# Kernel tuning notes

Measured on AMD Instinct MI355X. Metric: run time of the kernel, lower is better.

Reference implementation:

```python
import jax, jax.numpy as jnp
import numpy as np
import math

B, L, CS, CZ, H = 1, 256, 384, 128, 8
DH_S = CS // H
NEG = -1e9

def _ln(x, g, b):
    m = x.mean(-1, keepdims=True)
    v = ((x - m) ** 2).mean(-1, keepdims=True)
    return (x - m) / jnp.sqrt(v + 1e-5) * g + b

def _mha(x, mask, w_in, b_in, w_out, b_out):
    # torch nn.MultiheadAttention (batch_first) with packed in_proj [3C,C]
    N, Lx, C = x.shape
    dh = C // H
    qkv = x @ w_in.T + b_in
    q, k, v = jnp.split(qkv, 3, axis=-1)
    q = q.reshape(N, Lx, H, dh)
    k = k.reshape(N, Lx, H, dh)
    v = v.reshape(N, Lx, H, dh)
    logits = jnp.einsum('nlhd,nmhd->nhlm', q, k) / math.sqrt(dh)
    logits = jnp.where(mask[:, None, None, :], logits, NEG)
    a = jax.nn.softmax(logits, axis=-1)
    o = jnp.einsum('nhlm,nmhd->nlhd', a, v).reshape(N, Lx, C)
    return o @ w_out.T + b_out

def _forward(s, z, s_norm_g, s_norm_b, z_norm_g, z_norm_b, wq, bq, wk, bk, wv, bv, wzb, bzb, wo, bo, sff_w1, sff_b1, sff_w2, sff_b2, pz_norm_g, pz_norm_b, row_in_w, row_in_b, row_out_w, row_out_b, col_in_w, col_in_b, col_out_w, col_out_b, szi_w, szj_w, zff_w1, zff_b1, zff_w2, zff_b2, pair_mask):
    Bx, Lx, _ = s.shape
    # --- pair-bias attention on s ---
    sn = _ln(s, s_norm_g, s_norm_b)
    zn = _ln(z, z_norm_g, z_norm_b)
    q = (sn @ wq + bq).reshape(Bx, Lx, H, DH_S)
    k = (sn @ wk + bk).reshape(Bx, Lx, H, DH_S)
    v = (sn @ wv + bv).reshape(Bx, Lx, H, DH_S)
    logits = jnp.einsum('blhd,bmhd->bhlm', q, k) / math.sqrt(DH_S)
    logits = logits + jnp.transpose(zn @ wzb + bzb, (0, 3, 1, 2))
    logits = jnp.where(pair_mask[:, None, :, :], logits, NEG)
    attn = jax.nn.softmax(logits, axis=-1)
    o = jnp.einsum('bhlm,bmhd->blhd', attn, v).reshape(Bx, Lx, CS)
    s = s + o @ wo + bo
    # --- s feedforward ---
    sn = _ln(s, s_norm_g, s_norm_b)
    s = s + jax.nn.gelu(sn @ sff_w1 + sff_b1, approximate=False) @ sff_w2 + sff_b2
    # --- pair row/col attention ---
    znp = _ln(z, pz_norm_g, pz_norm_b)
    z_row = znp.reshape(Bx * Lx, Lx, CZ)
    row_out = _mha(z_row, pair_mask.reshape(Bx * Lx, Lx), row_in_w, row_in_b, row_out_w, row_out_b).reshape(Bx, Lx, Lx, CZ)
    z_col = jnp.transpose(znp, (0, 2, 1, 3)).reshape(Bx * Lx, Lx, CZ)
    col_mask = jnp.transpose(pair_mask, (0, 2, 1)).reshape(Bx * Lx, Lx)
    col_out = _mha(z_col, col_mask, col_in_w, col_in_b, col_out_w, col_out_b).reshape(Bx, Lx, Lx, CZ)
    col_out = jnp.transpose(col_out, (0, 2, 1, 3))
    z = z + row_out + col_out
    # --- outer-sum update from s ---
    sn = _ln(s, s_norm_g, s_norm_b)
    z = z + (sn @ szi_w)[:, :, None, :] + (sn @ szj_w)[:, None, :, :]
    # --- z feedforward (reuses z_norm as in source) ---
    znf = _ln(z, z_norm_g, z_norm_b)
    z = z + jax.nn.gelu(znf @ zff_w1 + zff_b1, approximate=False) @ zff_w2 + zff_b2
    return s, z

def setup_inputs():
    ks = iter(jax.random.split(jax.random.key(0), 64))
    def rn(sh, sc=0.02):
        return jax.random.normal(next(ks), sh, jnp.float32) * sc
    d = {}
    d['s'] = jax.random.normal(next(ks), (B, L, CS), jnp.float32)
    d['z'] = jax.random.normal(next(ks), (B, L, L, CZ), jnp.float32)
    d['pair_mask'] = jnp.ones((B, L, L), dtype=bool)
    d['s_norm_g'] = jnp.ones((CS,), jnp.float32); d['s_norm_b'] = jnp.zeros((CS,), jnp.float32)
    d['z_norm_g'] = jnp.ones((CZ,), jnp.float32); d['z_norm_b'] = jnp.zeros((CZ,), jnp.float32)
    d['wq'] = rn((CS, CS)); d['bq'] = jnp.zeros((CS,), jnp.float32)
    d['wk'] = rn((CS, CS)); d['bk'] = jnp.zeros((CS,), jnp.float32)
    d['wv'] = rn((CS, CS)); d['bv'] = jnp.zeros((CS,), jnp.float32)
    d['wzb'] = rn((CZ, H)); d['bzb'] = jnp.zeros((H,), jnp.float32)
    d['wo'] = rn((CS, CS)); d['bo'] = jnp.zeros((CS,), jnp.float32)
    d['sff_w1'] = rn((CS, 4 * CS)); d['sff_b1'] = jnp.zeros((4 * CS,), jnp.float32)
    d['sff_w2'] = rn((4 * CS, CS)); d['sff_b2'] = jnp.zeros((CS,), jnp.float32)
    d['pz_norm_g'] = jnp.ones((CZ,), jnp.float32); d['pz_norm_b'] = jnp.zeros((CZ,), jnp.float32)
    d['row_in_w'] = rn((3 * CZ, CZ)); d['row_in_b'] = jnp.zeros((3 * CZ,), jnp.float32)
    d['row_out_w'] = rn((CZ, CZ)); d['row_out_b'] = jnp.zeros((CZ,), jnp.float32)
    d['col_in_w'] = rn((3 * CZ, CZ)); d['col_in_b'] = jnp.zeros((3 * CZ,), jnp.float32)
    d['col_out_w'] = rn((CZ, CZ)); d['col_out_b'] = jnp.zeros((CZ,), jnp.float32)
    d['szi_w'] = rn((CS, CZ)); d['szj_w'] = rn((CS, CZ))
    d['zff_w1'] = rn((CZ, 4 * CZ)); d['zff_b1'] = jnp.zeros((4 * CZ,), jnp.float32)
    d['zff_w2'] = rn((4 * CZ, CZ)); d['zff_b2'] = jnp.zeros((CZ,), jnp.float32)
    return d

def reference(s, z, pair_mask, s_norm_g, s_norm_b, z_norm_g, z_norm_b, wq, bq, wk, bk, wv, bv, wzb, bzb, wo, bo, sff_w1, sff_b1, sff_w2, sff_b2, pz_norm_g, pz_norm_b, row_in_w, row_in_b, row_out_w, row_out_b, col_in_w, col_in_b, col_out_w, col_out_b, szi_w, szj_w, zff_w1, zff_b1, zff_w2, zff_b2):
    return _forward(s, z, s_norm_g, s_norm_b, z_norm_g, z_norm_b, wq, bq, wk, bk, wv, bv, wzb, bzb, wo, bo, sff_w1, sff_b1, sff_w2, sff_b2, pz_norm_g, pz_norm_b, row_in_w, row_in_b, row_out_w, row_out_b, col_in_w, col_in_b, col_out_w, col_out_b, szi_w, szj_w, zff_w1, zff_b1, zff_w2, zff_b2, pair_mask)
```

## Files before the change

kernel.cpp:

```cpp
#include <hip/hip_runtime.h>
#include <math.h>

#define LL 256
#define CSD 384
#define CZD 128
#define HNUM 8
#define DHS 48
#define DHZ 16

typedef __bf16 bf16_t;
typedef bf16_t bf16x8 __attribute__((ext_vector_type(8)));
typedef float f32x4 __attribute__((ext_vector_type(4)));
typedef float f32x16 __attribute__((ext_vector_type(16)));

template <typename OUT>
__global__ void ln_kernel(const float* __restrict__ x, const float* __restrict__ g,
                          const float* __restrict__ b, OUT* __restrict__ y, int W) {
    size_t row = blockIdx.x;
    int t = threadIdx.x;
    float v = x[row * (size_t)W + t];
    float s = v, s2 = v * v;
#pragma unroll
    for (int o = 32; o > 0; o >>= 1) { s += __shfl_down(s, o); s2 += __shfl_down(s2, o); }
    __shared__ float sh[8], sh2[8];
    int w = t >> 6, nw = W >> 6;
    if ((t & 63) == 0) { sh[w] = s; sh2[w] = s2; }
    __syncthreads();
    if (t == 0) {
        float a = 0, a2 = 0;
        for (int i = 0; i < nw; i++) { a += sh[i]; a2 += sh2[i]; }
        sh[0] = a; sh2[0] = a2;
    }
    __syncthreads();
    float mean = sh[0] / W;
    float var = sh2[0] / W - mean * mean;
    y[row * (size_t)W + t] = (OUT)((v - mean) * rsqrtf(var + 1e-5f) * g[t] + b[t]);
}

__global__ __launch_bounds__(256) void zlnbias_kernel(
        const float* __restrict__ z, const float* __restrict__ zng, const float* __restrict__ znb,
        const float* __restrict__ pzg, const float* __restrict__ pzb,
        const float* __restrict__ wzb, const float* __restrict__ bzb,
        float* __restrict__ bias, bf16_t* __restrict__ znp) {
    __shared__ float swzb[1024];
    int tid = threadIdx.x;
    *(float4*)&swzb[tid * 4] = *(const float4*)&wzb[tid * 4];
    __syncthreads();
    int p = blockIdx.x * 32 + (tid >> 3);
    int g = tid & 7, c0 = g * 16;
    const float* row = z + (size_t)p * 128 + c0;
    float v[16];
#pragma unroll
    for (int i = 0; i < 4; i++) *(float4*)&v[i * 4] = *(const float4*)(row + i * 4);
    float s = 0.f, s2 = 0.f;
#pragma unroll
    for (int c = 0; c < 16; c++) { s += v[c]; s2 += v[c] * v[c]; }
#pragma unroll
    for (int m = 1; m <= 4; m <<= 1) { s += __shfl_xor(s, m); s2 += __shfl_xor(s2, m); }
    float mean = s * 0.0078125f;
    float var = s2 * 0.0078125f - mean * mean;
    float rstd = rsqrtf(var + 1e-5f);
    float zg[16], zb[16], pg[16], pb[16];
#pragma unroll
    for (int i = 0; i < 4; i++) {
        *(float4*)&zg[i * 4] = *(const float4*)(zng + c0 + i * 4);
        *(float4*)&zb[i * 4] = *(const float4*)(znb + c0 + i * 4);
        *(float4*)&pg[i * 4] = *(const float4*)(pzg + c0 + i * 4);
        *(float4*)&pb[i * 4] = *(const float4*)(pzb + c0 + i * 4);
    }
    float pr[8] = {0.f, 0.f, 0.f, 0.f, 0.f, 0.f, 0.f, 0.f};
    bf16_t ob[16];
#pragma unroll
    for (int c = 0; c < 16; c++) {
        float nrm = (v[c] - mean) * rstd;
        ob[c] = (bf16_t)(nrm * pg[c] + pb[c]);
        float zn = nrm * zg[c] + zb[c];
        float4 w0 = *(const float4*)&swzb[(c0 + c) * 8];
        float4 w1 = *(const float4*)&swzb[(c0 + c) * 8 + 4];
        pr[0] += zn * w0.x; pr[1] += zn * w0.y; pr[2] += zn * w0.z; pr[3] += zn * w0.w;
        pr[4] += zn * w1.x; pr[5] += zn * w1.y; pr[6] += zn * w1.z; pr[7] += zn * w1.w;
    }
    bf16_t* orow = znp + (size_t)p * 128 + c0;
    *(uint4*)orow = *(uint4*)&ob[0];
    *(uint4*)(orow + 8) = *(uint4*)&ob[8];
#pragma unroll
    for (int m = 1; m <= 4; m <<= 1)
#pragma unroll
        for (int h = 0; h < 8; h++) pr[h] += __shfl_xor(pr[h], m);
    if (g == 0) {
#pragma unroll
        for (int h = 0; h < 8; h++) bias[(size_t)h * 65536 + p] = pr[h] + bzb[h];
    }
}

__global__ __launch_bounds__(256) void outerln_kernel(
        float* __restrict__ z, const float* __restrict__ ab,
        const float* __restrict__ zng, const float* __restrict__ znb,
        bf16_t* __restrict__ znp) {
    int tid = threadIdx.x;
    int p = blockIdx.x * 32 + (tid >> 3);
    int g = tid & 7, c0 = g * 16;
    int i = p >> 8, j = p & 255;
    float* row = z + (size_t)p * 128 + c0;
    float v[16];
#pragma unroll
    for (int q = 0; q < 4; q++) {
        float4 xv = *(const float4*)(row + q * 4);
        float4 av = *(const float4*)(ab + (size_t)i * 256 + c0 + q * 4);
        float4 bv = *(const float4*)(ab + (size_t)j * 256 + 128 + c0 + q * 4);
        v[q * 4 + 0] = xv.x + av.x + bv.x;
        v[q * 4 + 1] = xv.y + av.y + bv.y;
        v[q * 4 + 2] = xv.z + av.z + bv.z;
        v[q * 4 + 3] = xv.w + av.w + bv.w;
        *(float4*)(row + q * 4) = *(float4*)&v[q * 4];
    }
    float s = 0.f, s2 = 0.f;
#pragma unroll
    for (int c = 0; c < 16; c++) { s += v[c]; s2 += v[c] * v[c]; }
#pragma unroll
    for (int m = 1; m <= 4; m <<= 1) { s += __shfl_xor(s, m); s2 += __shfl_xor(s2, m); }
    float mean = s * 0.0078125f;
    float var = s2 * 0.0078125f - mean * mean;
    float rstd = rsqrtf(var + 1e-5f);
    float zg[16], zb[16];
#pragma unroll
    for (int q = 0; q < 4; q++) {
        *(float4*)&zg[q * 4] = *(const float4*)(zng + c0 + q * 4);
        *(float4*)&zb[q * 4] = *(const float4*)(znb + c0 + q * 4);
    }
    bf16_t ob[16];
#pragma unroll
    for (int c = 0; c < 16; c++) ob[c] = (bf16_t)((v[c] - mean) * rstd * zg[c] + zb[c]);
    bf16_t* orow = znp + (size_t)p * 128 + c0;
    *(uint4*)orow = *(uint4*)&ob[0];
    *(uint4*)(orow + 8) = *(uint4*)&ob[8];
}

__global__ void sattn_kernel(const float* __restrict__ qkv, const float* __restrict__ bias,
                             bf16_t* __restrict__ o) {
    int l = blockIdx.x, h = blockIdx.y;
    int m = threadIdx.x;
    const float* qr = qkv + (size_t)l * 1152 + h * DHS;
    const float* kr = qkv + (size_t)m * 1152 + 384 + h * DHS;
    float acc = 0.f;
#pragma unroll
    for (int d = 0; d < DHS; d++) acc += qr[d] * kr[d];
    acc = acc * 0.14433756729740643f + bias[(size_t)h * 65536 + l * 256 + m];

    __shared__ float attn[256];
    __shared__ float redm[4], reds[4];
    float x = acc;
#pragma unroll
    for (int off = 32; off > 0; off >>= 1) x = fmaxf(x, __shfl_down(x, off));
    if ((m & 63) == 0) redm[m >> 6] = x;
    __syncthreads();
    float mx = fmaxf(fmaxf(redm[0], redm[1]), fmaxf(redm[2], redm[3]));
    float p = __expf(acc - mx);
    float ss = p;
#pragma unroll
    for (int off = 32; off > 0; off >>= 1) ss += __shfl_down(ss, off);
    if ((m & 63) == 0) reds[m >> 6] = ss;
    __syncthreads();
    float sum = reds[0] + reds[1] + reds[2] + reds[3];
    attn[m] = p / sum;
    __syncthreads();
    if (m < DHS) {
        float a = 0.f;
        for (int j = 0; j < 256; j++) a += attn[j] * qkv[(size_t)j * 1152 + 768 + h * DHS + m];
        o[(size_t)l * CSD + h * DHS + m] = (bf16_t)a;
    }
}

__global__ __launch_bounds__(256) void pattn_mfma_kernel(const bf16_t* __restrict__ qkv,
                                                         bf16_t* __restrict__ o) {
    int n = blockIdx.x, h = blockIdx.y;
    int tid = threadIdx.x;
    __shared__ bf16_t Qs[256 * 24];
    __shared__ bf16_t Ks[256 * 24];
    __shared__ bf16_t Vt[32 * 264];
    __shared__ bf16_t Ps[4][32 * 72];

    {
        const bf16_t* row = qkv + ((size_t)n * 256 + tid) * 384 + h * 16;
        uint4 q0 = *(const uint4*)(row);
        uint4 q1 = *(const uint4*)(row + 8);
        uint4 k0 = *(const uint4*)(row + 128);
        uint4 k1 = *(const uint4*)(row + 136);
        uint4 v0 = *(const uint4*)(row + 256);
        uint4 v1 = *(const uint4*)(row + 264);
        *(uint4*)&Qs[tid * 24] = q0; *(uint4*)&Qs[tid * 24 + 8] = q1;
        *(uint4*)&Ks[tid * 24] = k0; *(uint4*)&Ks[tid * 24 + 8] = k1;
        bf16_t vv[16];
        *(uint4*)&vv[0] = v0; *(uint4*)&vv[8] = v1;
#pragma unroll
        for (int d = 0; d < 16; d++) Vt[d * 264 + tid] = vv[d];
        Vt[16 * 264 + tid] = (bf16_t)1.0f;
    }
    __syncthreads();

    int wv = tid >> 6, lane = tid & 63;
    int l5 = lane >> 5, l31 = lane & 31;
    bf16_t* P = &Ps[wv][0];
    const f32x16 zero16 = {0.f,0.f,0.f,0.f,0.f,0.f,0.f,0.f,0.f,0.f,0.f,0.f,0.f,0.f,0.f,0.f};

    for (int chunk = 0; chunk < 2; chunk++) {
        int q0i = wv * 64 + chunk * 32;
        bf16x8 aq = *(const bf16x8*)&Qs[(q0i + l31) * 24 + l5 * 8];
        f32x16 oacc = zero16;
        for (int kt = 0; kt < 4; kt++) {
#pragma unroll
            for (int ct2 = 0; ct2 < 2; ct2++) {
                int ct = kt * 2 + ct2;
                bf16x8 kb = *(const bf16x8*)&Ks[(ct * 32 + l31) * 24 + l5 * 8];
                f32x16 s = __builtin_amdgcn_mfma_f32_32x32x16_bf16(aq, kb, zero16, 0, 0, 0);
#pragma unroll
                for (int r = 0; r < 16; r++) {
                    float p = __expf(0.25f * s[r]);
                    int prow = (r & 3) + 8 * (r >> 2) + 4 * l5;
                    P[prow * 72 + ct2 * 32 + l31] = (bf16_t)p;
                }
            }
#pragma unroll
            for (int st = 0; st < 4; st++) {
                bf16x8 pa = *(const bf16x8*)&P[l31 * 72 + st * 16 + l5 * 8];
                bf16x8 vb = *(const bf16x8*)&Vt[l31 * 264 + kt * 64 + st * 16 + l5 * 8];
                oacc = __builtin_amdgcn_mfma_f32_32x32x16_bf16(pa, vb, oacc, 0, 0, 0);
            }
        }
#pragma unroll
        for (int r = 0; r < 16; r++) {
            float v = oacc[r];
            float sum = __shfl(v, (lane & 32) + 16, 64);
            int prow = (r & 3) + 8 * (r >> 2) + 4 * l5;
            if (l31 < 16)
                o[((size_t)n * 256 + q0i + prow) * CZD + h * 16 + l31] = (bf16_t)(v / sum);
        }
    }
}

template <int RES, int ACT, int OUTBF>
__global__ __launch_bounds__(256) void sgemm_kernel(const bf16_t* __restrict__ A,
                                                    const bf16_t* __restrict__ Bw,
                                                    const float* __restrict__ bias,
                                                    const float* __restrict__ R,
                                                    float* __restrict__ C,
                                                    bf16_t* __restrict__ Cb,
                                                    int M, int N, int K) {
    __shared__ bf16_t As[2][64 * 72];
    __shared__ bf16_t Bs[2][64 * 72];
    int tid = threadIdx.x;
    int bm = blockIdx.y * 64, bn = blockIdx.x * 64;
    int lane = tid & 63, wv = tid >> 6;
    int wm = (wv >> 1) * 32, wn = (wv & 1) * 32;
    int lrow = lane & 15, lchunk = lane >> 4;
    int r0 = tid >> 2, c0 = (tid & 3) * 16;

    f32x4 acc[2][2];
#pragma unroll
    for (int i = 0; i < 2; i++)
#pragma unroll
        for (int j = 0; j < 2; j++) acc[i][j] = (f32x4){0.f, 0.f, 0.f, 0.f};

    size_t sa = (size_t)(bm + r0) * K + c0;
    size_t sb = (size_t)(bn + r0) * K + c0;
    uint4 a0 = *(const uint4*)(A + sa);
    uint4 a1 = *(const uint4*)(A + sa + 8);
    uint4 b0 = *(const uint4*)(Bw + sb);
    uint4 b1 = *(const uint4*)(Bw + sb + 8);

    int iters = K >> 6;
    for (int it = 0; it < iters; it++) {
        bf16_t* Aw = &As[it & 1][0];
        bf16_t* Bww = &Bs[it & 1][0];
        *(uint4*)&Aw[r0 * 72 + c0] = a0;
        *(uint4*)&Aw[r0 * 72 + c0 + 8] = a1;
        *(uint4*)&Bww[r0 * 72 + c0] = b0;
        *(uint4*)&Bww[r0 * 72 + c0 + 8] = b1;
        __syncthreads();
        if (it + 1 < iters) {
            size_t oa = sa + (size_t)(it + 1) * 64;
            size_t ob = sb + (size_t)(it + 1) * 64;
            a0 = *(const uint4*)(A + oa);
            a1 = *(const uint4*)(A + oa + 8);
            b0 = *(const uint4*)(Bw + ob);
            b1 = *(const uint4*)(Bw + ob + 8);
        }
#pragma unroll
        for (int ki = 0; ki < 2; ki++) {
            bf16x8 af[2], bfr[2];
#pragma unroll
            for (int f = 0; f < 2; f++) {
                af[f] = *(const bf16x8*)&Aw[(wm + f * 16 + lrow) * 72 + ki * 32 + lchunk * 8];
                bfr[f] = *(const bf16x8*)&Bww[(wn + f * 16 + lrow) * 72 + ki * 32 + lchunk * 8];
            }
#pragma unroll
            for (int fi = 0; fi < 2; fi++)
#pragma unroll
                for (int fj = 0; fj < 2; fj++)
                    acc[fi][fj] = __builtin_amdgcn_mfma_f32_16x16x32_bf16(af[fi], bfr[fj], acc[fi][fj], 0, 0, 0);
        }
        __syncthreads();
    }
#pragma unroll
    for (int fi = 0; fi < 2; fi++) {
#pragma unroll
        for (int i = 0; i < 4; i++) {
            int gm = bm + wm + fi * 16 + lchunk * 4 + i;
            size_t crow = (size_t)gm * N;
#pragma unroll
            for (int fj = 0; fj < 2; fj++) {
                int gn = bn + wn + fj * 16 + lrow;
                float val = acc[fi][fj][i];
                if (bias) val += bias[gn];
                if (ACT == 1) val = 0.5f * val * (1.f + erff(val * 0.70710678118654752f));
                if (RES == 2) val += R[crow + gn];
                if (OUTBF) Cb[crow + gn] = (bf16_t)val;
                else C[crow + gn] = val;
            }
        }
    }
}

template <int APERM, int RES, int ACT, int OUTBF>
__global__ __launch_bounds__(256) void mgemm_kernel(const bf16_t* __restrict__ A,
                                                    const bf16_t* __restrict__ Bw,
                                                    const float* __restrict__ bias,
                                                    const float* __restrict__ R,
                                                    float* __restrict__ C,
                                                    bf16_t* __restrict__ Cb,
                                                    int M, int N, int K) {
    __shared__ bf16_t As[128 * 40];
    __shared__ bf16_t Bs[128 * 40];
    int tid = threadIdx.x;
    int bm = blockIdx.y * 128, bn = blockIdx.x * 128;
    int lane = tid & 63, wvid = tid >> 6;
    int wm = (wvid >> 1) * 64, wn = (wvid & 1) * 64;
    int lrow = lane & 15, lchunk = lane >> 4;

    f32x4 acc[4][4];
#pragma unroll
    for (int i = 0; i < 4; i++)
#pragma unroll
        for (int j = 0; j < 4; j++) acc[i][j] = (f32x4){0.f, 0.f, 0.f, 0.f};

    int r0 = tid >> 2, c0 = tid & 3;
    int ra0 = bm + r0, ra1 = bm + r0 + 64;
    if (APERM) {
        ra0 = ((ra0 & 255) << 8) | (ra0 >> 8);
        ra1 = ((ra1 & 255) << 8) | (ra1 >> 8);
    }
    size_t sa0 = (size_t)ra0 * K, sa1 = (size_t)ra1 * K;
    size_t sb0 = (size_t)(bn + r0) * K, sb1 = (size_t)(bn + r0 + 64) * K;

    for (int k0 = 0; k0 < K; k0 += 32) {
        uint4 va0 = *(const uint4*)(A + sa0 + k0 + c0 * 8);
        uint4 va1 = *(const uint4*)(A + sa1 + k0 + c0 * 8);
        uint4 vb0 = *(const uint4*)(Bw + sb0 + k0 + c0 * 8);
        uint4 vb1 = *(const uint4*)(Bw + sb1 + k0 + c0 * 8);
        __syncthreads();
        *(uint4*)&As[r0 * 40 + c0 * 8] = va0;
        *(uint4*)&As[(r0 + 64) * 40 + c0 * 8] = va1;
        *(uint4*)&Bs[r0 * 40 + c0 * 8] = vb0;
        *(uint4*)&Bs[(r0 + 64) * 40 + c0 * 8] = vb1;
        __syncthreads();
        bf16x8 af[4], bfr[4];
#pragma unroll
        for (int f = 0; f < 4; f++) {
            af[f] = *(const bf16x8*)&As[(wm + f * 16 + lrow) * 40 + lchunk * 8];
            bfr[f] = *(const bf16x8*)&Bs[(wn + f * 16 + lrow) * 40 + lchunk * 8];
        }
#pragma unroll
        for (int fi = 0; fi < 4; fi++)
#pragma unroll
            for (int fj = 0; fj < 4; fj++)
                acc[fi][fj] = __builtin_amdgcn_mfma_f32_16x16x32_bf16(af[fi], bfr[fj], acc[fi][fj], 0, 0, 0);
    }
#pragma unroll
    for (int fi = 0; fi < 4; fi++) {
#pragma unroll
        for (int i = 0; i < 4; i++) {
            int gm = bm + wm + fi * 16 + lchunk * 4 + i;
            size_t crow = (size_t)gm * N;
#pragma unroll
            for (int fj = 0; fj < 4; fj++) {
                int gn = bn + wn + fj * 16 + lrow;
                float val = acc[fi][fj][i];
                if (bias) val += bias[gn];
                if (ACT == 1) val = 0.5f * val * (1.f + erff(val * 0.70710678118654752f));
                if (RES == 1) val += C[crow + gn];
                else if (RES == 2) val += R[crow + gn];
                if (OUTBF) Cb[crow + gn] = (bf16_t)val;
                else C[crow + gn] = val;
            }
        }
    }
}

struct PrepArgs {
    const float *wq, *wk, *wv, *wo, *sffw1, *sffw2, *szi, *szj, *zffw1, *zffw2;
    const float *rinw, *cinw, *routw, *coutw, *bq, *bk, *bv;
    bf16_t *wqkv, *wwo, *wsf1, *wsf2, *wszij, *wzf1, *wzf2;
    bf16_t *wrin, *wcin, *wrout, *wcout;
    float* biasqkv;
};
__device__ inline void dev_trans(const float* in, bf16_t* out, int i, int N, int K) {
    int k = i / N, n = i % N;
    out[(size_t)n * K + k] = (bf16_t)in[i];
}
__global__ void prep_kernel(PrepArgs a) {
    int i = blockIdx.x * 256 + threadIdx.x;
    if (i < 147456) { dev_trans(a.wq, a.wqkv, i, 384, 384); return; }
    i -= 147456;
    if (i < 147456) { dev_trans(a.wk, a.wqkv + 384 * 384, i, 384, 384); return; }
    i -= 147456;
    if (i < 147456) { dev_trans(a.wv, a.wqkv + 768 * 384, i, 384, 384); return; }
    i -= 147456;
    if (i < 147456) { dev_trans(a.wo, a.wwo, i, 384, 384); return; }
    i -= 147456;
    if (i < 589824) { dev_trans(a.sffw1, a.wsf1, i, 1536, 384); return; }
    i -= 589824;
    if (i < 589824) { dev_trans(a.sffw2, a.wsf2, i, 384, 1536); return; }
    i -= 589824;
    if (i < 49152) { dev_trans(a.szi, a.wszij, i, 128, 384); return; }
    i -= 49152;
    if (i < 49152) { dev_trans(a.szj, a.wszij + 128 * 384, i, 128, 384); return; }
    i -= 49152;
    if (i < 65536) { dev_trans(a.zffw1, a.wzf1, i, 512, 128); return; }
    i -= 65536;
    if (i < 65536) { dev_trans(a.zffw2, a.wzf2, i, 128, 512); return; }
    i -= 65536;
    if (i < 49152) { a.wrin[i] = (bf16_t)a.rinw[i]; return; }
    i -= 49152;
    if (i < 49152) { a.wcin[i] = (bf16_t)a.cinw[i]; return; }
    i -= 49152;
    if (i < 16384) { a.wrout[i] = (bf16_t)a.routw[i]; return; }
    i -= 16384;
    if (i < 16384) { a.wcout[i] = (bf16_t)a.coutw[i]; return; }
    i -= 16384;
    if (i < 384) { a.biasqkv[i] = a.bq[i]; return; }
    i -= 384;
    if (i < 384) { a.biasqkv[384 + i] = a.bk[i]; return; }
    i -= 384;
    if (i < 384) { a.biasqkv[768 + i] = a.bv[i]; return; }
}

extern "C" void kernel_launch(void* const* d_in, const int* in_sizes, int n_in,
                              void* d_out, int out_size, void* d_ws, size_t ws_size,
                              hipStream_t stream) {
    const float* s_in = (const float*)d_in[0];
    const float* z_in = (const float*)d_in[1];
    const float* sng = (const float*)d_in[3];
    const float* snb = (const float*)d_in[4];
    const float* zng = (const float*)d_in[5];
    const float* znb = (const float*)d_in[6];
    const float* wq = (const float*)d_in[7];
    const float* bq = (const float*)d_in[8];
    const float* wk = (const float*)d_in[9];
    const float* bk = (const float*)d_in[10];
    const float* wv = (const float*)d_in[11];
    const float* bv = (const float*)d_in[12];
    const float* wzb = (const float*)d_in[13];
    const float* bzb = (const float*)d_in[14];
    const float* wo = (const float*)d_in[15];
    const float* bo = (const float*)d_in[16];
    const float* sffw1 = (const float*)d_in[17];
    const float* sffb1 = (const float*)d_in[18];
    const float* sffw2 = (const float*)d_in[19];
    const float* sffb2 = (const float*)d_in[20];
    const float* pzg = (const float*)d_in[21];
    const float* pzb = (const float*)d_in[22];
    const float* rinw = (const float*)d_in[23];
    const float* rinb = (const float*)d_in[24];
    const float* routw = (const float*)d_in[25];
    const float* routb = (const float*)d_in[26];
    const float* cinw = (const float*)d_in[27];
    const float* cinb = (const float*)d_in[28];
    const float* coutw = (const float*)d_in[29];
    const float* coutb = (const float*)d_in[30];
    const float* sziw = (const float*)d_in[31];
    const float* szjw = (const float*)d_in[32];
    const float* zffw1 = (const float*)d_in[33];
    const float* zffb1 = (const float*)d_in[34];
    const float* zffw2 = (const float*)d_in[35];
    const float* zffb2 = (const float*)d_in[36];

    float* ws = (float*)d_ws;
    bf16_t* qkvbf = (bf16_t*)ws;
    bf16_t* hbf = (bf16_t*)ws;
    float* obregion = ws + 25165824;
    bf16_t* obbf = (bf16_t*)obregion;
    bf16_t* znpbf = (bf16_t*)(ws + 29360128);
    bf16_t* snbf = (bf16_t*)obregion;
    float* qkv_s = obregion + 49152;
    float* biasb = obregion + 344064;
    bf16_t* osbf = (bf16_t*)(obregion + 868352);
    float* s1 = obregion + 917504;
    bf16_t* sn2bf = (bf16_t*)(obregion + 1015808);
    bf16_t* hsbf = (bf16_t*)(obregion + 1064960);
    bf16_t* wrin = (bf16_t*)(ws + 33554432);
    bf16_t* wcin = (bf16_t*)(ws + 33579008);
    bf16_t* wrout = (bf16_t*)(ws + 33603584);
    bf16_t* wcout = (bf16_t*)(ws + 33611776);
    bf16_t* wzf1 = (bf16_t*)(ws + 33619968);
    bf16_t* wzf2 = (bf16_t*)(ws + 33652736);
    bf16_t* wqkv = (bf16_t*)(ws + 33685504);
    bf16_t* wwo = (bf16_t*)(ws + 33906688);
    bf16_t* wsf1 = (bf16_t*)(ws + 33980416);
    bf16_t* wsf2 = (bf16_t*)(ws + 34275328);
    bf16_t* wszij = (bf16_t*)(ws + 34570240);
    float* biasqkv = ws + 34619392;
    bf16_t* sn3bf = (bf16_t*)(ws + 34620544);
    float* ab = ws + 34669696;

    float* sout = (float*)d_out;
    float* zout = sout + 98304;

    dim3 b256(256);

    PrepArgs pa;
    pa.wq = wq; pa.wk = wk; pa.wv = wv; pa.wo = wo;
    pa.sffw1 = sffw1; pa.sffw2 = sffw2; pa.szi = sziw; pa.szj = szjw;
    pa.zffw1 = zffw1; pa.zffw2 = zffw2;
    pa.rinw = rinw; pa.cinw = cinw; pa.routw = routw; pa.coutw = coutw;
    pa.bq = bq; pa.bk = bk; pa.bv = bv;
    pa.wqkv = wqkv; pa.wwo = wwo; pa.wsf1 = wsf1; pa.wsf2 = wsf2; pa.wszij = wszij;
    pa.wzf1 = wzf1; pa.wzf2 = wzf2;
    pa.wrin = wrin; pa.wcin = wcin; pa.wrout = wrout; pa.wcout = wcout;
    pa.biasqkv = biasqkv;
    prep_kernel<<<dim3(8329), b256, 0, stream>>>(pa);

    zlnbias_kernel<<<dim3(2048), b256, 0, stream>>>(z_in, zng, znb, pzg, pzb, wzb, bzb, biasb, znpbf);

    ln_kernel<bf16_t><<<dim3(LL), dim3(CSD), 0, stream>>>(s_in, sng, snb, snbf, CSD);
    sgemm_kernel<0, 0, 0><<<dim3(18, 4), b256, 0, stream>>>(snbf, wqkv, biasqkv, nullptr, qkv_s, nullptr, 256, 1152, 384);
    sattn_kernel<<<dim3(LL, HNUM), b256, 0, stream>>>(qkv_s, biasb, osbf);
    sgemm_kernel<2, 0, 0><<<dim3(6, 4), b256, 0, stream>>>(osbf, wwo, bo, s_in, s1, nullptr, 256, 384, 384);
    ln_kernel<bf16_t><<<dim3(LL), dim3(CSD), 0, stream>>>(s1, sng, snb, sn2bf, CSD);
    sgemm_kernel<0, 1, 1><<<dim3(24, 4), b256, 0, stream>>>(sn2bf, wsf1, sffb1, nullptr, nullptr, hsbf, 256, 1536, 384);
    sgemm_kernel<2, 0, 0><<<dim3(6, 4), b256, 0, stream>>>(hsbf, wsf2, sffb2, s1, sout, nullptr, 256, 384, 1536);
    ln_kernel<bf16_t><<<dim3(LL), dim3(CSD), 0, stream>>>(sout, sng, snb, sn3bf, CSD);
    sgemm_kernel<0, 0, 0><<<dim3(4, 4), b256, 0, stream>>>(sn3bf, wszij, nullptr, nullptr, ab, nullptr, 256, 256, 384);
    mgemm_kernel<0, 0, 0, 1><<<dim3(3, 512), b256, 0, stream>>>(znpbf, wrin, rinb, nullptr, nullptr, qkvbf, 65536, 384, CZD);
    pattn_mfma_kernel<<<dim3(256, HNUM), b256, 0, stream>>>(qkvbf, obbf);
    mgemm_kernel<0, 2, 0, 0><<<dim3(1, 512), b256, 0, stream>>>(obbf, wrout, routb, z_in, zout, nullptr, 65536, CZD, CZD);
    mgemm_kernel<1, 0, 0, 1><<<dim3(3, 512), b256, 0, stream>>>(znpbf, wcin, cinb, nullptr, nullptr, qkvbf, 65536, 384, CZD);
    pattn_mfma_kernel<<<dim3(256, HNUM), b256, 0, stream>>>(qkvbf, obbf);
    mgemm_kernel<1, 1, 0, 0><<<dim3(1, 512), b256, 0, stream>>>(obbf, wcout, coutb, nullptr, zout, nullptr, 65536, CZD, CZD);
    outerln_kernel<<<dim3(2048), b256, 0, stream>>>(zout, ab, zng, znb, znpbf);
    mgemm_kernel<0, 0, 1, 1><<<dim3(4, 512), b256, 0, stream>>>(znpbf, wzf1, zffb1, nullptr, nullptr, hbf, 65536, 512, CZD);
    mgemm_kernel<0, 1, 0, 0><<<dim3(1, 512), b256, 0, stream>>>(hbf, wzf2, zffb2, nullptr, zout, nullptr, 65536, CZD, 512);
}
```

Measured before the change: 629.7 us.

## Fuse col-out GEMM with outer-product add and LayerNorm, and fuse the z feedforward

The column-attention output projection, the outer-product update of z and the following LayerNorm now run in one kernel. It stages the output tile in shared memory and computes row statistics there. The z feedforward's two GEMMs are fused so the GELU hidden activations stay in shared memory and are never written to or read back from global memory. This removes several full passes over the 65536x128 pair tensor and the 65536x512 hidden buffer. In exchange, the fused FFN kernel uses more shared memory per block and reloads the weight chunks per block, which may lower occupancy.

New measurement: 591.3 us. -6.1%, faster.

```diff
diff --git a/kernel.cpp b/kernel.cpp
--- a/kernel.cpp
+++ b/kernel.cpp
@@ -91,49 +91,6 @@
 #pragma unroll
         for (int h = 0; h < 8; h++) bias[(size_t)h * 65536 + p] = pr[h] + bzb[h];
     }
-}
-
-__global__ __launch_bounds__(256) void outerln_kernel(
-        float* __restrict__ z, const float* __restrict__ ab,
-        const float* __restrict__ zng, const float* __restrict__ znb,
-        bf16_t* __restrict__ znp) {
-    int tid = threadIdx.x;
-    int p = blockIdx.x * 32 + (tid >> 3);
-    int g = tid & 7, c0 = g * 16;
-    int i = p >> 8, j = p & 255;
-    float* row = z + (size_t)p * 128 + c0;
-    float v[16];
-#pragma unroll
-    for (int q = 0; q < 4; q++) {
-        float4 xv = *(const float4*)(row + q * 4);
-        float4 av = *(const float4*)(ab + (size_t)i * 256 + c0 + q * 4);
-        float4 bv = *(const float4*)(ab + (size_t)j * 256 + 128 + c0 + q * 4);
-        v[q * 4 + 0] = xv.x + av.x + bv.x;
-        v[q * 4 + 1] = xv.y + av.y + bv.y;
-        v[q * 4 + 2] = xv.z + av.z + bv.z;
-        v[q * 4 + 3] = xv.w + av.w + bv.w;
-        *(float4*)(row + q * 4) = *(float4*)&v[q * 4];
-    }
-    float s = 0.f, s2 = 0.f;
-#pragma unroll
-    for (int c = 0; c < 16; c++) { s += v[c]; s2 += v[c] * v[c]; }
-#pragma unroll
-    for (int m = 1; m <= 4; m <<= 1) { s += __shfl_xor(s, m); s2 += __shfl_xor(s2, m); }
-    float mean = s * 0.0078125f;
-    float var = s2 * 0.0078125f - mean * mean;
-    float rstd = rsqrtf(var + 1e-5f);
-    float zg[16], zb[16];
-#pragma unroll
-    for (int q = 0; q < 4; q++) {
-        *(float4*)&zg[q * 4] = *(const float4*)(zng + c0 + q * 4);
-        *(float4*)&zb[q * 4] = *(const float4*)(znb + c0 + q * 4);
-    }
-    bf16_t ob[16];
-#pragma unroll
-    for (int c = 0; c < 16; c++) ob[c] = (bf16_t)((v[c] - mean) * rstd * zg[c] + zb[c]);
-    bf16_t* orow = znp + (size_t)p * 128 + c0;
-    *(uint4*)orow = *(uint4*)&ob[0];
-    *(uint4*)(orow + 8) = *(uint4*)&ob[8];
 }
 
 __global__ void sattn_kernel(const float* __restrict__ qkv, const float* __restrict__ bias,
@@ -392,6 +349,191 @@
                 if (OUTBF) Cb[crow + gn] = (bf16_t)val;
                 else C[crow + gn] = val;
             }
+        }
+    }
+}
+
+__global__ __launch_bounds__(256) void colout_fused_kernel(
+        const bf16_t* __restrict__ A, const bf16_t* __restrict__ Bw,
+        const float* __restrict__ bias, const float* __restrict__ ab,
+        const float* __restrict__ zng, const float* __restrict__ znb,
+        float* __restrict__ z, bf16_t* __restrict__ znp) {
+    __shared__ __align__(16) char smem[128 * 129 * 4];
+    bf16_t* As = (bf16_t*)smem;
+    bf16_t* Bs = (bf16_t*)(smem + 10240);
+    float* lnb = (float*)smem;
+    int tid = threadIdx.x;
+    int bm = blockIdx.x * 128;
+    int lane = tid & 63, wvid = tid >> 6;
+    int wm = (wvid >> 1) * 64, wn = (wvid & 1) * 64;
+    int lrow = lane & 15, lchunk = lane >> 4;
+
+    f32x4 acc[4][4];
+#pragma unroll
+    for (int i = 0; i < 4; i++)
+#pragma unroll
+        for (int j = 0; j < 4; j++) acc[i][j] = (f32x4){0.f, 0.f, 0.f, 0.f};
+
+    int r0 = tid >> 2, c0 = tid & 3;
+    int ra0 = bm + r0, ra1 = bm + r0 + 64;
+    ra0 = ((ra0 & 255) << 8) | (ra0 >> 8);
+    ra1 = ((ra1 & 255) << 8) | (ra1 >> 8);
+    size_t sa0 = (size_t)ra0 * 128, sa1 = (size_t)ra1 * 128;
+    size_t sb0 = (size_t)r0 * 128, sb1 = (size_t)(r0 + 64) * 128;
+
+    for (int k0 = 0; k0 < 128; k0 += 32) {
+        uint4 va0 = *(const uint4*)(A + sa0 + k0 + c0 * 8);
+        uint4 va1 = *(const uint4*)(A + sa1 + k0 + c0 * 8);
+        uint4 vb0 = *(const uint4*)(Bw + sb0 + k0 + c0 * 8);
+        uint4 vb1 = *(const uint4*)(Bw + sb1 + k0 + c0 * 8);
+        __syncthreads();
+        *(uint4*)&As[r0 * 40 + c0 * 8] = va0;
+        *(uint4*)&As[(r0 + 64) * 40 + c0 * 8] = va1;
+        *(uint4*)&Bs[r0 * 40 + c0 * 8] = vb0;
+        *(uint4*)&Bs[(r0 + 64) * 40 + c0 * 8] = vb1;
+        __syncthreads();
+        bf16x8 af[4], bfr[4];
+#pragma unroll
+        for (int f = 0; f < 4; f++) {
+            af[f] = *(const bf16x8*)&As[(wm + f * 16 + lrow) * 40 + lchunk * 8];
+            bfr[f] = *(const bf16x8*)&Bs[(wn + f * 16 + lrow) * 40 + lchunk * 8];
+        }
+#pragma unroll
+        for (int fi = 0; fi < 4; fi++)
+#pragma unroll
+            for (int fj = 0; fj < 4; fj++)
+                acc[fi][fj] = __builtin_amdgcn_mfma_f32_16x16x32_bf16(af[fi], bfr[fj], acc[fi][fj], 0, 0, 0);
+    }
+    __syncthreads();
+#pragma unroll
+    for (int fi = 0; fi < 4; fi++) {
+#pragma unroll
+        for (int i = 0; i < 4; i++) {
+            int lm = wm + fi * 16 + lchunk * 4 + i;
+            int gm = bm + lm;
+            int irow = gm >> 8, jcol = gm & 255;
+            size_t crow = (size_t)gm * 128;
+#pragma unroll
+            for (int fj = 0; fj < 4; fj++) {
+                int gn = wn + fj * 16 + lrow;
+                float val = acc[fi][fj][i] + bias[gn] + z[crow + gn]
+                          + ab[(size_t)irow * 256 + gn] + ab[(size_t)jcol * 256 + 128 + gn];
+                z[crow + gn] = val;
+                lnb[lm * 129 + gn] = val;
+            }
+        }
+    }
+    __syncthreads();
+    {
+        int r = tid >> 1, half = tid & 1;
+        const float* rowp = &lnb[r * 129 + half * 64];
+        float s = 0.f, s2 = 0.f;
+#pragma unroll
+        for (int q = 0; q < 64; q++) { float v = rowp[q]; s += v; s2 += v * v; }
+        s += __shfl_xor(s, 1); s2 += __shfl_xor(s2, 1);
+        float mean = s * 0.0078125f;
+        float rstd = rsqrtf(s2 * 0.0078125f - mean * mean + 1e-5f);
+        int gm = bm + r;
+        bf16_t ob[64];
+#pragma unroll
+        for (int q = 0; q < 64; q++)
+            ob[q] = (bf16_t)((rowp[q] - mean) * rstd * zng[half * 64 + q] + znb[half * 64 + q]);
+        bf16_t* orow = znp + (size_t)gm * 128 + half * 64;
+#pragma unroll
+        for (int q = 0; q < 8; q++) *(uint4*)(orow + q * 8) = *(uint4*)&ob[q * 8];
+    }
+}
+
+__global__ __launch_bounds__(256) void zff_fused_kernel(
+        const bf16_t* __restrict__ znp, const bf16_t* __restrict__ w1,
+        const bf16_t* __restrict__ w2,
+        const float* __restrict__ b1, const float* __restrict__ b2,
+        float* __restrict__ z) {
+    __shared__ bf16_t Azn[64 * 136];
+    __shared__ bf16_t Wbuf[128 * 136];
+    __shared__ bf16_t Hbuf[4][16 * 136];
+    int tid = threadIdx.x;
+    int lane = tid & 63, wv = tid >> 6;
+    int lrow = lane & 15, lchunk = lane >> 4;
+    int r0 = blockIdx.x * 64;
+
+    {
+        int ar = tid >> 2;
+        int ac = (tid & 3) * 32;
+        const bf16_t* src = znp + (size_t)(r0 + ar) * 128 + ac;
+#pragma unroll
+        for (int q = 0; q < 4; q++)
+            *(uint4*)&Azn[ar * 136 + ac + q * 8] = *(const uint4*)(src + q * 8);
+    }
+
+    f32x4 acc2[8];
+#pragma unroll
+    for (int j = 0; j < 8; j++) acc2[j] = (f32x4){0.f, 0.f, 0.f, 0.f};
+
+    bf16_t* H = &Hbuf[wv][0];
+    for (int nc = 0; nc < 4; nc++) {
+        __syncthreads();
+        {
+            int wr = tid >> 1;
+            int wc = (tid & 1) * 64;
+            const bf16_t* src = w1 + (size_t)(nc * 128 + wr) * 128 + wc;
+#pragma unroll
+            for (int q = 0; q < 8; q++)
+                *(uint4*)&Wbuf[wr * 136 + wc + q * 8] = *(const uint4*)(src + q * 8);
+        }
+        __syncthreads();
+        f32x4 acc1[8];
+#pragma unroll
+        for (int j = 0; j < 8; j++) acc1[j] = (f32x4){0.f, 0.f, 0.f, 0.f};
+#pragma unroll
+        for (int ki = 0; ki < 4; ki++) {
+            bf16x8 a = *(const bf16x8*)&Azn[(wv * 16 + lrow) * 136 + ki * 32 + lchunk * 8];
+#pragma unroll
+            for (int fj = 0; fj < 8; fj++) {
+                bf16x8 b = *(const bf16x8*)&Wbuf[(fj * 16 + lrow) * 136 + ki * 32 + lchunk * 8];
+                acc1[fj] = __builtin_amdgcn_mfma_f32_16x16x32_bf16(a, b, acc1[fj], 0, 0, 0);
+            }
+        }
+#pragma unroll
+        for (int fj = 0; fj < 8; fj++) {
+            int col = fj * 16 + lrow;
+            float bb = b1[nc * 128 + col];
+#pragma unroll
+            for (int ii = 0; ii < 4; ii++) {
+                float v = acc1[fj][ii] + bb;
+                v = 0.5f * v * (1.f + erff(v * 0.70710678118654752f));
+                H[(lchunk * 4 + ii) * 136 + col] = (bf16_t)v;
+            }
+        }
+        __syncthreads();
+        {
+            int wr = tid >> 1;
+            int wc = (tid & 1) * 64;
+            const bf16_t* src = w2 + (size_t)wr * 512 + nc * 128 + wc;
+#pragma unroll
+            for (int q = 0; q < 8; q++)
+                *(uint4*)&Wbuf[wr * 136 + wc + q * 8] = *(const uint4*)(src + q * 8);
+        }
+        __syncthreads();
+#pragma unroll
+        for (int ki = 0; ki < 4; ki++) {
+            bf16x8 a = *(const bf16x8*)&H[lrow * 136 + ki * 32 + lchunk * 8];
+#pragma unroll
+            for (int fj = 0; fj < 8; fj++) {
+                bf16x8 b = *(const bf16x8*)&Wbuf[(fj * 16 + lrow) * 136 + ki * 32 + lchunk * 8];
+                acc2[fj] = __builtin_amdgcn_mfma_f32_16x16x32_bf16(a, b, acc2[fj], 0, 0, 0);
+            }
+        }
+    }
+#pragma unroll
+    for (int fj = 0; fj < 8; fj++) {
+        int col = fj * 16 + lrow;
+        float bb = b2[col];
+#pragma unroll
+        for (int ii = 0; ii < 4; ii++) {
+            int grow = r0 + wv * 16 + lchunk * 4 + ii;
+            size_t idx = (size_t)grow * 128 + col;
+            z[idx] += acc2[fj][ii] + bb;
         }
     }
 }
@@ -486,7 +628,6 @@
 
     float* ws = (float*)d_ws;
     bf16_t* qkvbf = (bf16_t*)ws;
-    bf16_t* hbf = (bf16_t*)ws;
     float* obregion = ws + 25165824;
     bf16_t* obbf = (bf16_t*)obregion;
     bf16_t* znpbf = (bf16_t*)(ws + 29360128);
@@ -545,8 +686,6 @@
     mgemm_kernel<0, 2, 0, 0><<<dim3(1, 512), b256, 0, stream>>>(obbf, wrout, routb, z_in, zout, nullptr, 65536, CZD, CZD);
     mgemm_kernel<1, 0, 0, 1><<<dim3(3, 512), b256, 0, stream>>>(znpbf, wcin, cinb, nullptr, nullptr, qkvbf, 65536, 384, CZD);
     pattn_mfma_kernel<<<dim3(256, HNUM), b256, 0, stream>>>(qkvbf, obbf);
-    mgemm_kernel<1, 1, 0, 0><<<dim3(1, 512), b256, 0, stream>>>(obbf, wcout, coutb, nullptr, zout, nullptr, 65536, CZD, CZD);
-    outerln_kernel<<<dim3(2048), b256, 0, stream>>>(zout, ab, zng, znb, znpbf);
-    mgemm_kernel<0, 0, 1, 1><<<dim3(4, 512), b256, 0, stream>>>(znpbf, wzf1, zffb1, nullptr, nullptr, hbf, 65536, 512, CZD);
-    mgemm_kernel<0, 1, 0, 0><<<dim3(1, 512), b256, 0, stream>>>(hbf, wzf2, zffb2, nullptr, zout, nullptr, 65536, CZD, 512);
-}
+    colout_fused_kernel<<<dim3(512), b256, 0, stream>>>(obbf, wcout, coutb, ab, zng, znb, zout, znpbf);
+    zff_fused_kernel<<<dim3(1024), b256, 0, stream>>>(znpbf, wzf1, wzf2, zffb1, zffb2, zout);
+}
```

## Fuse col-attention out-projection with outer-sum add and LayerNorm; use full-K GEMM tiles

Applied to the files above, without the earlier changes.

The col-attention output GEMM now also adds the outer-sum terms and runs the pair LayerNorm in its epilogue. Rows are staged through shared memory, so the separate outerln pass and its extra read/write of z go away. The pair GEMMs switch to a kernel that loads a 128-wide K chunk at once and issues four MFMA k-steps per sync, with fewer barriers and loads. The trade is much larger shared-memory use (about 68 KB per block), which may lower occupancy.

New measurement: 653.5 us. 1.04x slower.

```diff
diff --git a/kernel.cpp b/kernel.cpp
--- a/kernel.cpp
+++ b/kernel.cpp
@@ -91,49 +91,6 @@
 #pragma unroll
         for (int h = 0; h < 8; h++) bias[(size_t)h * 65536 + p] = pr[h] + bzb[h];
     }
-}
-
-__global__ __launch_bounds__(256) void outerln_kernel(
-        float* __restrict__ z, const float* __restrict__ ab,
-        const float* __restrict__ zng, const float* __restrict__ znb,
-        bf16_t* __restrict__ znp) {
-    int tid = threadIdx.x;
-    int p = blockIdx.x * 32 + (tid >> 3);
-    int g = tid & 7, c0 = g * 16;
-    int i = p >> 8, j = p & 255;
-    float* row = z + (size_t)p * 128 + c0;
-    float v[16];
-#pragma unroll
-    for (int q = 0; q < 4; q++) {
-        float4 xv = *(const float4*)(row + q * 4);
-        float4 av = *(const float4*)(ab + (size_t)i * 256 + c0 + q * 4);
-        float4 bv = *(const float4*)(ab + (size_t)j * 256 + 128 + c0 + q * 4);
-        v[q * 4 + 0] = xv.x + av.x + bv.x;
-        v[q * 4 + 1] = xv.y + av.y + bv.y;
-        v[q * 4 + 2] = xv.z + av.z + bv.z;
-        v[q * 4 + 3] = xv.w + av.w + bv.w;
-        *(float4*)(row + q * 4) = *(float4*)&v[q * 4];
-    }
-    float s = 0.f, s2 = 0.f;
-#pragma unroll
-    for (int c = 0; c < 16; c++) { s += v[c]; s2 += v[c] * v[c]; }
-#pragma unroll
-    for (int m = 1; m <= 4; m <<= 1) { s += __shfl_xor(s, m); s2 += __shfl_xor(s2, m); }
-    float mean = s * 0.0078125f;
-    float var = s2 * 0.0078125f - mean * mean;
-    float rstd = rsqrtf(var + 1e-5f);
-    float zg[16], zb[16];
-#pragma unroll
-    for (int q = 0; q < 4; q++) {
-        *(float4*)&zg[q * 4] = *(const float4*)(zng + c0 + q * 4);
-        *(float4*)&zb[q * 4] = *(const float4*)(znb + c0 + q * 4);
-    }
-    bf16_t ob[16];
-#pragma unroll
-    for (int c = 0; c < 16; c++) ob[c] = (bf16_t)((v[c] - mean) * rstd * zg[c] + zb[c]);
-    bf16_t* orow = znp + (size_t)p * 128 + c0;
-    *(uint4*)orow = *(uint4*)&ob[0];
-    *(uint4*)(orow + 8) = *(uint4*)&ob[8];
 }
 
 __global__ void sattn_kernel(const float* __restrict__ qkv, const float* __restrict__ bias,
@@ -321,16 +278,17 @@
     }
 }
 
-template <int APERM, int RES, int ACT, int OUTBF>
-__global__ __launch_bounds__(256) void mgemm_kernel(const bf16_t* __restrict__ A,
+template <int KTILES, int APERM, int RES, int ACT, int OUTBF>
+__global__ __launch_bounds__(256) void kgemm_kernel(const bf16_t* __restrict__ A,
                                                     const bf16_t* __restrict__ Bw,
                                                     const float* __restrict__ bias,
                                                     const float* __restrict__ R,
                                                     float* __restrict__ C,
                                                     bf16_t* __restrict__ Cb,
-                                                    int M, int N, int K) {
-    __shared__ bf16_t As[128 * 40];
-    __shared__ bf16_t Bs[128 * 40];
+                                                    int M, int N) {
+    const int K = KTILES * 128;
+    __shared__ bf16_t As[128 * 136];
+    __shared__ bf16_t Bs[128 * 136];
     int tid = threadIdx.x;
     int bm = blockIdx.y * 128, bn = blockIdx.x * 128;
     int lane = tid & 63, wvid = tid >> 6;
@@ -343,37 +301,38 @@
 #pragma unroll
         for (int j = 0; j < 4; j++) acc[i][j] = (f32x4){0.f, 0.f, 0.f, 0.f};
 
-    int r0 = tid >> 2, c0 = tid & 3;
-    int ra0 = bm + r0, ra1 = bm + r0 + 64;
-    if (APERM) {
-        ra0 = ((ra0 & 255) << 8) | (ra0 >> 8);
-        ra1 = ((ra1 & 255) << 8) | (ra1 >> 8);
-    }
-    size_t sa0 = (size_t)ra0 * K, sa1 = (size_t)ra1 * K;
-    size_t sb0 = (size_t)(bn + r0) * K, sb1 = (size_t)(bn + r0 + 64) * K;
-
-    for (int k0 = 0; k0 < K; k0 += 32) {
-        uint4 va0 = *(const uint4*)(A + sa0 + k0 + c0 * 8);
-        uint4 va1 = *(const uint4*)(A + sa1 + k0 + c0 * 8);
-        uint4 vb0 = *(const uint4*)(Bw + sb0 + k0 + c0 * 8);
-        uint4 vb1 = *(const uint4*)(Bw + sb1 + k0 + c0 * 8);
+    int r0 = tid >> 1, half = (tid & 1) * 64;
+    int ra = bm + r0;
+    if (APERM) ra = ((ra & 255) << 8) | (ra >> 8);
+    const bf16_t* Abase = A + (size_t)ra * K + half;
+    const bf16_t* Bbase = Bw + (size_t)(bn + r0) * K + half;
+    bf16_t* Ad = &As[r0 * 136 + half];
+    bf16_t* Bd = &Bs[r0 * 136 + half];
+
+    for (int kc = 0; kc < KTILES; kc++) {
+        if (KTILES > 1 && kc > 0) __syncthreads();
+#pragma unroll
+        for (int q = 0; q < 8; q++) {
+            uint4 av = *(const uint4*)(Abase + kc * 128 + q * 8);
+            uint4 bv = *(const uint4*)(Bbase + kc * 128 + q * 8);
+            *(uint4*)(Ad + q * 8) = av;
+            *(uint4*)(Bd + q * 8) = bv;
+        }
         __syncthreads();
-        *(uint4*)&As[r0 * 40 + c0 * 8] = va0;
-        *(uint4*)&As[(r0 + 64) * 40 + c0 * 8] = va1;
-        *(uint4*)&Bs[r0 * 40 + c0 * 8] = vb0;
-        *(uint4*)&Bs[(r0 + 64) * 40 + c0 * 8] = vb1;
-        __syncthreads();
-        bf16x8 af[4], bfr[4];
-#pragma unroll
-        for (int f = 0; f < 4; f++) {
-            af[f] = *(const bf16x8*)&As[(wm + f * 16 + lrow) * 40 + lchunk * 8];
-            bfr[f] = *(const bf16x8*)&Bs[(wn + f * 16 + lrow) * 40 + lchunk * 8];
-        }
-#pragma unroll
-        for (int fi = 0; fi < 4; fi++)
-#pragma unroll
-            for (int fj = 0; fj < 4; fj++)
-                acc[fi][fj] = __builtin_amdgcn_mfma_f32_16x16x32_bf16(af[fi], bfr[fj], acc[fi][fj], 0, 0, 0);
+#pragma unroll
+        for (int ki = 0; ki < 4; ki++) {
+            bf16x8 af[4], bfr[4];
+#pragma unroll
+            for (int f = 0; f < 4; f++) {
+                af[f] = *(const bf16x8*)&As[(wm + f * 16 + lrow) * 136 + ki * 32 + lchunk * 8];
+                bfr[f] = *(const bf16x8*)&Bs[(wn + f * 16 + lrow) * 136 + ki * 32 + lchunk * 8];
+            }
+#pragma unroll
+            for (int fi = 0; fi < 4; fi++)
+#pragma unroll
+                for (int fj = 0; fj < 4; fj++)
+                    acc[fi][fj] = __builtin_amdgcn_mfma_f32_16x16x32_bf16(af[fi], bfr[fj], acc[fi][fj], 0, 0, 0);
+        }
     }
 #pragma unroll
     for (int fi = 0; fi < 4; fi++) {
@@ -393,6 +352,92 @@
                 else C[crow + gn] = val;
             }
         }
+    }
+}
+
+__global__ __launch_bounds__(256) void colout_fused_kernel(
+        const bf16_t* __restrict__ A, const bf16_t* __restrict__ Bw,
+        const float* __restrict__ bias, const float* __restrict__ ab,
+        const float* __restrict__ zng, const float* __restrict__ znb,
+        float* __restrict__ z, bf16_t* __restrict__ znp) {
+    __shared__ __align__(16) char smem[2 * 128 * 136 * 2];
+    bf16_t* As = (bf16_t*)smem;
+    bf16_t* Bs = (bf16_t*)(smem + 128 * 136 * 2);
+    float* lnb = (float*)smem;
+    int tid = threadIdx.x;
+    int bm = blockIdx.x * 128;
+    int lane = tid & 63, wvid = tid >> 6;
+    int wm = (wvid >> 1) * 64, wn = (wvid & 1) * 64;
+    int lrow = lane & 15, lchunk = lane >> 4;
+
+    f32x4 acc[4][4];
+#pragma unroll
+    for (int i = 0; i < 4; i++)
+#pragma unroll
+        for (int j = 0; j < 4; j++) acc[i][j] = (f32x4){0.f, 0.f, 0.f, 0.f};
+
+    int r0 = tid >> 1, half = (tid & 1) * 64;
+    int ra = bm + r0;
+    ra = ((ra & 255) << 8) | (ra >> 8);
+#pragma unroll
+    for (int q = 0; q < 8; q++) {
+        uint4 av = *(const uint4*)(A + (size_t)ra * 128 + half + q * 8);
+        uint4 bv = *(const uint4*)(Bw + (size_t)r0 * 128 + half + q * 8);
+        *(uint4*)&As[r0 * 136 + half + q * 8] = av;
+        *(uint4*)&Bs[r0 * 136 + half + q * 8] = bv;
+    }
+    __syncthreads();
+#pragma unroll
+    for (int ki = 0; ki < 4; ki++) {
+        bf16x8 af[4], bfr[4];
+#pragma unroll
+        for (int f = 0; f < 4; f++) {
+            af[f] = *(const bf16x8*)&As[(wm + f * 16 + lrow) * 136 + ki * 32 + lchunk * 8];
+            bfr[f] = *(const bf16x8*)&Bs[(wn + f * 16 + lrow) * 136 + ki * 32 + lchunk * 8];
+        }
+#pragma unroll
+        for (int fi = 0; fi < 4; fi++)
+#pragma unroll
+            for (int fj = 0; fj < 4; fj++)
+                acc[fi][fj] = __builtin_amdgcn_mfma_f32_16x16x32_bf16(af[fi], bfr[fj], acc[fi][fj], 0, 0, 0);
+    }
+    __syncthreads();
+#pragma unroll
+    for (int fi = 0; fi < 4; fi++) {
+#pragma unroll
+        for (int i = 0; i < 4; i++) {
+            int lm = wm + fi * 16 + lchunk * 4 + i;
+            int gm = bm + lm;
+            int irow = gm >> 8, jcol = gm & 255;
+            size_t crow = (size_t)gm * 128;
+#pragma unroll
+            for (int fj = 0; fj < 4; fj++) {
+                int gn = wn + fj * 16 + lrow;
+                float val = acc[fi][fj][i] + bias[gn] + z[crow + gn]
+                          + ab[(size_t)irow * 256 + gn] + ab[(size_t)jcol * 256 + 128 + gn];
+                z[crow + gn] = val;
+                lnb[lm * 129 + gn] = val;
+            }
+        }
+    }
+    __syncthreads();
+    {
+        int r = tid >> 1, hhalf = tid & 1;
+        const float* rowp = &lnb[r * 129 + hhalf * 64];
+        float s = 0.f, s2 = 0.f;
+#pragma unroll
+        for (int q = 0; q < 64; q++) { float v = rowp[q]; s += v; s2 += v * v; }
+        s += __shfl_xor(s, 1); s2 += __shfl_xor(s2, 1);
+        float mean = s * 0.0078125f;
+        float rstd = rsqrtf(s2 * 0.0078125f - mean * mean + 1e-5f);
+        int gm = bm + r;
+        bf16_t ob[64];
+#pragma unroll
+        for (int q = 0; q < 64; q++)
+            ob[q] = (bf16_t)((rowp[q] - mean) * rstd * zng[hhalf * 64 + q] + znb[hhalf * 64 + q]);
+        bf16_t* orow = znp + (size_t)gm * 128 + hhalf * 64;
+#pragma unroll
+        for (int q = 0; q < 8; q++) *(uint4*)(orow + q * 8) = *(uint4*)&ob[q * 8];
     }
 }
 
@@ -540,13 +585,12 @@
     sgemm_kernel<2, 0, 0><<<dim3(6, 4), b256, 0, stream>>>(hsbf, wsf2, sffb2, s1, sout, nullptr, 256, 384, 1536);
     ln_kernel<bf16_t><<<dim3(LL), dim3(CSD), 0, stream>>>(sout, sng, snb, sn3bf, CSD);
     sgemm_kernel<0, 0, 0><<<dim3(4, 4), b256, 0, stream>>>(sn3bf, wszij, nullptr, nullptr, ab, nullptr, 256, 256, 384);
-    mgemm_kernel<0, 0, 0, 1><<<dim3(3, 512), b256, 0, stream>>>(znpbf, wrin, rinb, nullptr, nullptr, qkvbf, 65536, 384, CZD);
+    kgemm_kernel<1, 0, 0, 0, 1><<<dim3(3, 512), b256, 0, stream>>>(znpbf, wrin, rinb, nullptr, nullptr, qkvbf, 65536, 384);
     pattn_mfma_kernel<<<dim3(256, HNUM), b256, 0, stream>>>(qkvbf, obbf);
-    mgemm_kernel<0, 2, 0, 0><<<dim3(1, 512), b256, 0, stream>>>(obbf, wrout, routb, z_in, zout, nullptr, 65536, CZD, CZD);
-    mgemm_kernel<1, 0, 0, 1><<<dim3(3, 512), b256, 0, stream>>>(znpbf, wcin, cinb, nullptr, nullptr, qkvbf, 65536, 384, CZD);
+    kgemm_kernel<1, 0, 2, 0, 0><<<dim3(1, 512), b256, 0, stream>>>(obbf, wrout, routb, z_in, zout, nullptr, 65536, 128);
+    kgemm_kernel<1, 1, 0, 0, 1><<<dim3(3, 512), b256, 0, stream>>>(znpbf, wcin, cinb, nullptr, nullptr, qkvbf, 65536, 384);
     pattn_mfma_kernel<<<dim3(256, HNUM), b256, 0, stream>>>(qkvbf, obbf);
-    mgemm_kernel<1, 1, 0, 0><<<dim3(1, 512), b256, 0, stream>>>(obbf, wcout, coutb, nullptr, zout, nullptr, 65536, CZD, CZD);
-    outerln_kernel<<<dim3(2048), b256, 0, stream>>>(zout, ab, zng, znb, znpbf);
-    mgemm_kernel<0, 0, 1, 1><<<dim3(4, 512), b256, 0, stream>>>(znpbf, wzf1, zffb1, nullptr, nullptr, hbf, 65536, 512, CZD);
-    mgemm_kernel<0, 1, 0, 0><<<dim3(1, 512), b256, 0, stream>>>(hbf, wzf2, zffb2, nullptr, zout, nullptr, 65536, CZD, 512);
-}
+    colout_fused_kernel<<<dim3(512), b256, 0, stream>>>(obbf, wcout, coutb, ab, zng, znb, zout, znpbf);
+    kgemm_kernel<1, 0, 0, 1, 1><<<dim3(4, 512), b256, 0, stream>>>(znpbf, wzf1, zffb1, nullptr, nullptr, hbf, 65536, 512);
+    kgemm_kernel<4, 0, 1, 0, 0><<<dim3(1, 512), b256, 0, stream>>>(hbf, wzf2, zffb2, nullptr, zout, nullptr, 65536, 128);
+}
```
